# Performance work log

Hardware: AMD Instinct MI355X
Metric: run time of the kernel (lower is better)

## Reference

```python
import jax, jax.numpy as jnp
import numpy as np

# ---- static config (Phi-3-small layer 0, blocksparse branch) ----
HIDDEN = 4096
N_HEADS = 32
N_KV = 8
HEAD_DIM = HIDDEN // N_HEADS        # 128
Q_PER_KV = N_HEADS // N_KV          # 4
SEQ = 2048
ROPE_BASE = 1000000.0
POS_SCALE = 1.0
SM_SCALE = 1.0 / HEAD_DIM           # mup scaling, multiplier=1.0
BLOCK = 64
LOCAL_BLOCKS = 16
VERT_STRIDE = 8


def _blocksparse_mask(seq_len):
    """Dense [S,S] bool mask realizing the causal blocksparse pattern:
    query block i attends key block j iff j<=i and (i-j < LOCAL_BLOCKS or (j+1) % VERT_STRIDE == 0),
    with elementwise causality inside blocks. Built once in numpy (static)."""
    nb = seq_len // BLOCK
    qb = np.arange(nb)[:, None]
    kb = np.arange(nb)[None, :]
    bmask = (kb <= qb) & ((qb - kb < LOCAL_BLOCKS) | ((kb + 1) % VERT_STRIDE == 0))
    emask = np.kron(bmask, np.ones((BLOCK, BLOCK), dtype=bool))
    i = np.arange(seq_len)
    emask &= i[:, None] >= i[None, :]
    return jnp.asarray(emask)


def _rope(x, cos, sin):
    # x: [B, S, H, D]; cos/sin: [S, D]
    x1, x2 = jnp.split(x, 2, axis=-1)
    rot = jnp.concatenate([-x2, x1], axis=-1)
    return x * cos[None, :, None, :] + rot * sin[None, :, None, :]


def setup_inputs() -> dict:
    key = jax.random.key(0)
    k1, k2, k3, k4, k5 = jax.random.split(key, 5)
    qkv_out = (N_HEADS + 2 * N_KV) * HEAD_DIM  # 6144
    return {
        "hidden_states": jax.random.normal(k1, (1, SEQ, HIDDEN), dtype=jnp.float32),
        "w_qkv": jax.random.normal(k2, (qkv_out, HIDDEN), dtype=jnp.float32) * 0.02,
        "b_qkv": jnp.zeros((qkv_out,), dtype=jnp.float32),
        "w_dense": jax.random.normal(k3, (HIDDEN, HIDDEN), dtype=jnp.float32) * 0.02,
        "b_dense": jnp.zeros((HIDDEN,), dtype=jnp.float32),
    }


def reference(hidden_states, w_qkv, b_qkv, w_dense, b_dense):
    B, S, _ = hidden_states.shape
    # grouped QKV projection: [B,S,(H+2*KV)*D]
    qkv = jnp.einsum("bsh,oh->bso", hidden_states, w_qkv) + b_qkv
    # group layout: (group, q0..q3, k, v) per kv head
    qkv = qkv.reshape(B, S, N_KV, Q_PER_KV + 2, HEAD_DIM)
    q = qkv[:, :, :, :Q_PER_KV].reshape(B, S, N_HEADS, HEAD_DIM)
    k = qkv[:, :, :, Q_PER_KV]   # [B,S,KV,D]
    v = qkv[:, :, :, Q_PER_KV + 1]
    # rotary embeddings (HF rotate-half style)
    inv_freq = 1.0 / (ROPE_BASE ** (jnp.arange(0, HEAD_DIM, 2, dtype=jnp.float32) / HEAD_DIM))
    t = jnp.arange(S, dtype=jnp.float32) * POS_SCALE
    freqs = jnp.outer(t, inv_freq)               # [S, D/2]
    emb = jnp.concatenate([freqs, freqs], axis=-1)
    cos, sin = jnp.cos(emb), jnp.sin(emb)
    q = _rope(q, cos, sin)
    k = _rope(k, cos, sin)
    # GQA: replicate kv heads to match q heads
    k = jnp.repeat(k, Q_PER_KV, axis=2)          # [B,S,H,D]
    v = jnp.repeat(v, Q_PER_KV, axis=2)
    mask = _blocksparse_mask(S)                  # [S,S] bool
    scores = jnp.einsum("bqhd,bkhd->bhqk", q, k) * SM_SCALE
    scores = jnp.where(mask[None, None], scores, jnp.finfo(scores.dtype).min)
    probs = jax.nn.softmax(scores, axis=-1)
    ctx = jnp.einsum("bhqk,bkhd->bqhd", probs, v).reshape(B, S, HIDDEN)
    out = jnp.einsum("bsh,oh->bso", ctx, w_dense) + b_dense
    return out
```

## Files before the change

### kernel.cpp

```cpp
#include <hip/hip_runtime.h>
#include <hip/hip_bf16.h>

#define SEQ 2048
#define HIDDEN 4096
#define NH 32
#define NKV 8
#define HD 128
#define QKV_OUT 6144
#define QSCALE (0.0078125f * 1.4426950408889634f)

typedef __attribute__((ext_vector_type(8))) short bf16x8;
typedef __attribute__((ext_vector_type(4))) float f32x4;
typedef __attribute__((ext_vector_type(16))) float f32x16;

__device__ inline unsigned short f32_bf16(float f) {
  union { float f; unsigned int u; } v; v.f = f;
  unsigned int r = v.u + 0x7FFFu + ((v.u >> 16) & 1u);
  return (unsigned short)(r >> 16);
}
__device__ inline float bf16_f32(unsigned short u) {
  union { unsigned int u; float f; } v; v.u = (unsigned int)u << 16;
  return v.f;
}
__device__ inline unsigned int pk(float a, float b) {
  union { __hip_bfloat162 h; unsigned int u; } t;
  t.h = __float22bfloat162_rn(make_float2(a, b));
  return t.u;
}
__device__ inline void pswap(unsigned int &a, unsigned int &b) {
  auto r = __builtin_amdgcn_permlane32_swap((int)a, (int)b, false, false);
  a = (unsigned int)r[0]; b = (unsigned int)r[1];
}
__device__ inline float xmax32(float v) {
  int x = __builtin_bit_cast(int, v);
  auto r = __builtin_amdgcn_permlane32_swap(x, x, false, false);
  return fmaxf(__builtin_bit_cast(float, (int)r[0]), __builtin_bit_cast(float, (int)r[1]));
}
__device__ inline float xadd32(float v) {
  int x = __builtin_bit_cast(int, v);
  auto r = __builtin_amdgcn_permlane32_swap(x, x, false, false);
  return __builtin_bit_cast(float, (int)r[0]) + __builtin_bit_cast(float, (int)r[1]);
}

__global__ __launch_bounds__(256) void conv_bf16(const float* __restrict__ in,
                                                 unsigned short* __restrict__ out,
                                                 int n) {
  int i = (blockIdx.x * 256 + threadIdx.x) * 8;
  if (i + 8 > n) return;
  float4 a = *reinterpret_cast<const float4*>(in + i);
  float4 b = *reinterpret_cast<const float4*>(in + i + 4);
  unsigned short t[8];
  t[0] = f32_bf16(a.x); t[1] = f32_bf16(a.y); t[2] = f32_bf16(a.z); t[3] = f32_bf16(a.w);
  t[4] = f32_bf16(b.x); t[5] = f32_bf16(b.y); t[6] = f32_bf16(b.z); t[7] = f32_bf16(b.w);
  *reinterpret_cast<uint4*>(out + i) = *reinterpret_cast<uint4*>(t);
}

__global__ __launch_bounds__(256) void build_tab(float* __restrict__ ct,
                                                 float* __restrict__ st) {
  int idx = blockIdx.x * 256 + threadIdx.x;
  int s = idx >> 6, d = idx & 63;
  float inv = powf(1.0e6f, -(float)d * (1.0f / 64.0f));
  float f = (float)s * inv;
  ct[idx] = cosf(f);
  st[idx] = sinf(f);
}

template <int BM, int CR, int CC, bool OBF>
__global__ __launch_bounds__(512, 2) void gemmF(const unsigned short* __restrict__ A,
                                                const unsigned short* __restrict__ B,
                                                const float* __restrict__ bias,
                                                void* __restrict__ Cp,
                                                int M, int N, int K) {
  constexpr int BN = 256;
  constexpr int MQ = BM / 64;
  constexpr int ABYT = BM * 128;
  constexpr int SB = ABYT + 32768;
  constexpr int NA = BM / 64;
  __shared__ __align__(16) char Lds[SB * 2];

  const int tid = threadIdx.x;
  const int wave = tid >> 6, lane = tid & 63;
  const int wr = wave >> 2, wc = wave & 3;
  const int lrow = lane & 15, lgrp = lane >> 4;

  const int ntx = N / BN;
  const int wg0 = blockIdx.x;
  const int xcd = wg0 & 7, w = wg0 >> 3;
  const int cpb = ntx / CC;
  const int band = xcd / cpb, colc = xcd % cpb;
  const int bm = (band * CR + w / CC) * BM;
  const int bn = (colc * CC + w % CC) * BN;

  const int r8 = lane >> 3;
  const int scol = ((lane & 7) ^ r8) * 8;
  const unsigned short* gA[NA]; int lA[NA];
#pragma unroll
  for (int j = 0; j < NA; ++j) {
    int row = bm + wave * (BM / 8) + j * 8 + r8;
    gA[j] = A + (size_t)row * K + scol;
    lA[j] = wave * (BM / 8) * 128 + j * 1024;
  }
  const unsigned short* gB[4]; int lB[4];
#pragma unroll
  for (int j = 0; j < 4; ++j) {
    int row = bn + wave * 32 + j * 8 + r8;
    gB[j] = B + (size_t)row * K + scol;
    lB[j] = ABYT + wave * 32 * 128 + j * 1024;
  }

  auto stage = [&](int t) {
    const int bufb = (t & 1) * SB;
    const int k0 = t * 64;
#pragma unroll
    for (int j = 0; j < NA; ++j)
      __builtin_amdgcn_global_load_lds(
          (const __attribute__((address_space(1))) unsigned int*)(gA[j] + k0),
          (__attribute__((address_space(3))) unsigned int*)(Lds + bufb + lA[j]), 16, 0, 0);
#pragma unroll
    for (int j = 0; j < 4; ++j)
      __builtin_amdgcn_global_load_lds(
          (const __attribute__((address_space(1))) unsigned int*)(gB[j] + k0),
          (__attribute__((address_space(3))) unsigned int*)(Lds + bufb + lB[j]), 16, 0, 0);
  };

  const int rsw = (lrow & 7) << 4;
  auto aoff = [&](int mh, int m, int ks) {
    return (wr * (BM / 2) + mh * (BM / 4) + m * 16 + lrow) * 128 +
           ((ks * 64 + lgrp * 16) ^ rsw);
  };
  auto boff = [&](int nh, int n, int ks) {
    return ABYT + (wc * 64 + nh * 32 + n * 16 + lrow) * 128 +
           ((ks * 64 + lgrp * 16) ^ rsw);
  };

  f32x4 acc[2 * MQ][4] = {};
  bf16x8 af[MQ][2], bf0[2][2], bf1[2][2];
  const int nt = K / 64;

  stage(0);
  asm volatile("s_waitcnt vmcnt(0)" ::: "memory");
  __builtin_amdgcn_sched_barrier(0);
  __builtin_amdgcn_s_barrier();
  __builtin_amdgcn_sched_barrier(0);

  for (int t = 0; t < nt; ++t) {
    const char* base = Lds + (t & 1) * SB;
    const bool pf = (t + 1) < nt;

    if (pf) stage(t + 1);
#pragma unroll
    for (int m = 0; m < MQ; ++m)
#pragma unroll
      for (int ks = 0; ks < 2; ++ks)
        af[m][ks] = *reinterpret_cast<const bf16x8*>(base + aoff(0, m, ks));
#pragma unroll
    for (int n = 0; n < 2; ++n)
#pragma unroll
      for (int ks = 0; ks < 2; ++ks)
        bf0[n][ks] = *reinterpret_cast<const bf16x8*>(base + boff(0, n, ks));
    __builtin_amdgcn_s_barrier();
    asm volatile("s_waitcnt lgkmcnt(0)" ::: "memory");
    __builtin_amdgcn_sched_barrier(0);
    __builtin_amdgcn_s_setprio(1);
#pragma unroll
    for (int m = 0; m < MQ; ++m)
#pragma unroll
      for (int n = 0; n < 2; ++n)
#pragma unroll
        for (int ks = 0; ks < 2; ++ks)
          acc[m][n] = __builtin_amdgcn_mfma_f32_16x16x32_bf16(af[m][ks], bf0[n][ks], acc[m][n], 0, 0, 0);
    __builtin_amdgcn_s_setprio(0);
    __builtin_amdgcn_s_barrier();

#pragma unroll
    for (int n = 0; n < 2; ++n)
#pragma unroll
      for (int ks = 0; ks < 2; ++ks)
        bf1[n][ks] = *reinterpret_cast<const bf16x8*>(base + boff(1, n, ks));
    __builtin_amdgcn_s_barrier();
    asm volatile("s_waitcnt lgkmcnt(0)" ::: "memory");
    __builtin_amdgcn_sched_barrier(0);
    __builtin_amdgcn_s_setprio(1);
#pragma unroll
    for (int m = 0; m < MQ; ++m)
#pragma unroll
      for (int n = 0; n < 2; ++n)
#pragma unroll
        for (int ks = 0; ks < 2; ++ks)
          acc[m][2 + n] = __builtin_amdgcn_mfma_f32_16x16x32_bf16(af[m][ks], bf1[n][ks], acc[m][2 + n], 0, 0, 0);
    __builtin_amdgcn_s_setprio(0);
    __builtin_amdgcn_s_barrier();

#pragma unroll
    for (int m = 0; m < MQ; ++m)
#pragma unroll
      for (int ks = 0; ks < 2; ++ks)
        af[m][ks] = *reinterpret_cast<const bf16x8*>(base + aoff(1, m, ks));
    __builtin_amdgcn_s_barrier();
    asm volatile("s_waitcnt lgkmcnt(0)" ::: "memory");
    __builtin_amdgcn_sched_barrier(0);
    __builtin_amdgcn_s_setprio(1);
#pragma unroll
    for (int m = 0; m < MQ; ++m)
#pragma unroll
      for (int n = 0; n < 2; ++n)
#pragma unroll
        for (int ks = 0; ks < 2; ++ks)
          acc[MQ + m][n] = __builtin_amdgcn_mfma_f32_16x16x32_bf16(af[m][ks], bf0[n][ks], acc[MQ + m][n], 0, 0, 0);
    __builtin_amdgcn_s_setprio(0);
    __builtin_amdgcn_s_barrier();

    __builtin_amdgcn_s_setprio(1);
#pragma unroll
    for (int m = 0; m < MQ; ++m)
#pragma unroll
      for (int n = 0; n < 2; ++n)
#pragma unroll
        for (int ks = 0; ks < 2; ++ks)
          acc[MQ + m][2 + n] = __builtin_amdgcn_mfma_f32_16x16x32_bf16(af[m][ks], bf1[n][ks], acc[MQ + m][2 + n], 0, 0, 0);
    __builtin_amdgcn_s_setprio(0);
    if (pf) {
      asm volatile("s_waitcnt vmcnt(0)" ::: "memory");
      __builtin_amdgcn_sched_barrier(0);
      __builtin_amdgcn_s_barrier();
      __builtin_amdgcn_sched_barrier(0);
    }
  }

#pragma unroll
  for (int ni = 0; ni < 4; ++ni) {
    int col = bn + wc * 64 + ni * 16 + lrow;
    float bv = bias[col];
#pragma unroll
    for (int mi = 0; mi < 2 * MQ; ++mi)
#pragma unroll
      for (int r = 0; r < 4; ++r) {
        int row = bm + wr * (BM / 2) + mi * 16 + lgrp * 4 + r;
        if constexpr (OBF)
          ((unsigned short*)Cp)[(size_t)row * N + col] = f32_bf16(acc[mi][ni][r] + bv);
        else
          ((float*)Cp)[(size_t)row * N + col] = acc[mi][ni][r] + bv;
      }
  }
}

__global__ __launch_bounds__(256) void rope_split(const unsigned short* __restrict__ qkvb,
                                                  const float* __restrict__ ct,
                                                  const float* __restrict__ st,
                                                  unsigned short* __restrict__ Q,
                                                  unsigned short* __restrict__ Kh,
                                                  unsigned short* __restrict__ Vt) {
  int b = blockIdx.x;
  if (b < 5120) {
    int t = b * 256 + threadIdx.x;
    int d8 = (t & 15) * 8;
    int q = t >> 4;
    int s = q / 40;
    int slotg = q - s * 40;
    int g = slotg / 5, slot = slotg - g * 5;
    const unsigned short* base = qkvb + (size_t)s * QKV_OUT + g * 768 + slot * 128;
    bf16x8 x8 = *reinterpret_cast<const bf16x8*>(base + d8);
    bf16x8 r8 = *reinterpret_cast<const bf16x8*>(base + (d8 ^ 64));
    float4 c0 = *reinterpret_cast<const float4*>(ct + s * 64 + (d8 & 63));
    float4 c1 = *reinterpret_cast<const float4*>(ct + s * 64 + (d8 & 63) + 4);
    float4 s0 = *reinterpret_cast<const float4*>(st + s * 64 + (d8 & 63));
    float4 s1 = *reinterpret_cast<const float4*>(st + s * 64 + (d8 & 63) + 4);
    float cc[8] = {c0.x, c0.y, c0.z, c0.w, c1.x, c1.y, c1.z, c1.w};
    float ss[8] = {s0.x, s0.y, s0.z, s0.w, s1.x, s1.y, s1.z, s1.w};
    float sgn = (d8 < 64) ? -1.0f : 1.0f;
    float sc = (slot < 4) ? QSCALE : 1.0f;
    unsigned short o[8];
#pragma unroll
    for (int i = 0; i < 8; ++i) {
      float x = bf16_f32((unsigned short)x8[i]);
      float r = bf16_f32((unsigned short)r8[i]) * sgn;
      o[i] = f32_bf16((x * cc[i] + r * ss[i]) * sc);
    }
    unsigned short* dst = (slot < 4)
        ? Q + ((size_t)(g * 4 + slot) * SEQ + s) * HD + d8
        : Kh + ((size_t)g * SEQ + s) * HD + d8;
    *reinterpret_cast<uint4*>(dst) = *reinterpret_cast<uint4*>(o);
  } else {
    int t2 = (b - 5120) * 256 + threadIdx.x;
    int d = t2 & 127;
    int rest = t2 >> 7;
    int g = rest & 7;
    int s0 = (rest >> 3) * 8;
    const unsigned short* src = qkvb + (size_t)s0 * QKV_OUT + g * 768 + 640 + d;
    unsigned short o[8];
#pragma unroll
    for (int i = 0; i < 8; ++i) o[i] = src[(size_t)i * QKV_OUT];
    *reinterpret_cast<uint4*>(&Vt[((size_t)g * HD + d) * SEQ + s0]) =
        *reinterpret_cast<uint4*>(o);
  }
}

__device__ inline int nextj(int x, int qb) {
  if (x > qb) return -1;
  if (qb - x < 16) return x;
  int v = (x & ~7) + 7;
  int w = qb - 15;
  return v < w ? v : w;
}

__global__ __launch_bounds__(256, 2) void attn32(const unsigned short* __restrict__ Q,
                                                 const unsigned short* __restrict__ Kh,
                                                 const unsigned short* __restrict__ Vt,
                                                 unsigned short* __restrict__ ctx) {
  const int g = blockIdx.x;
  const int y = (int)gridDim.y - 1 - (int)blockIdx.y;
  const int qb = y >> 1, half = y & 1;
  const int Q0 = y * 32;
  const int tid = threadIdx.x;
  const int wave = tid >> 6;
  const int h = g * 4 + wave;
  const int lane = tid & 63;
  const int l31 = lane & 31, hi = lane >> 5;

  __shared__ __align__(16) char Lds[65536];

  auto stage = [&](int bufb, int j) {
#pragma unroll
    for (int i = 0; i < 4; ++i) {
      int row = i * 16 + (tid >> 4);
      const unsigned short* src =
          Kh + ((size_t)(g * SEQ + j * 64 + row)) * HD + ((tid & 15) ^ (row & 15)) * 8;
      __builtin_amdgcn_global_load_lds(
          (const __attribute__((address_space(1))) unsigned int*)src,
          (__attribute__((address_space(3))) unsigned int*)(Lds + bufb + i * 4096 + (tid >> 6) * 1024),
          16, 0, 0);
    }
#pragma unroll
    for (int i = 0; i < 4; ++i) {
      int row = i * 32 + (tid >> 3);
      const unsigned short* src =
          Vt + ((size_t)(g * HD + row)) * SEQ + j * 64 + ((tid & 7) ^ (row & 7)) * 8;
      __builtin_amdgcn_global_load_lds(
          (const __attribute__((address_space(1))) unsigned int*)src,
          (__attribute__((address_space(3))) unsigned int*)(Lds + bufb + 16384 + i * 4096 + (tid >> 6) * 1024),
          16, 0, 0);
    }
  };

  bf16x8 qf[8];
  const unsigned short* qbase = Q + ((size_t)h * SEQ + Q0 + l31) * HD;
#pragma unroll
  for (int kk = 0; kk < 8; ++kk)
    qf[kk] = *reinterpret_cast<const bf16x8*>(qbase + kk * 16 + hi * 8);

  f32x16 ot[4] = {};
  float mrow = -1e30f, lsum = 0.f;

  const int kswz = l31 & 15;
  const int vswz = l31 & 7;

  int j = nextj(0, qb);
  int cur = 0;
  stage(0, j);
  asm volatile("s_waitcnt vmcnt(0)" ::: "memory");
  __builtin_amdgcn_sched_barrier(0);
  __builtin_amdgcn_s_barrier();
  __builtin_amdgcn_sched_barrier(0);

  while (true) {
    const int jn = (j < qb) ? nextj(j + 1, qb) : -1;
    if (jn >= 0) stage(cur ^ 32768, jn);

    const char* kb = Lds + cur;
    const char* vb = Lds + cur + 16384;
    const bool diag = (j == qb);
    const bool short_blk = diag && (half == 0);

    f32x16 st[2] = {};
    __builtin_amdgcn_s_setprio(1);
#pragma unroll
    for (int kk = 0; kk < 8; ++kk) {
      bf16x8 k0 = *reinterpret_cast<const bf16x8*>(
          kb + (size_t)l31 * 256 + (((2 * kk + hi) ^ kswz) * 16));
      st[0] = __builtin_amdgcn_mfma_f32_32x32x16_bf16(k0, qf[kk], st[0], 0, 0, 0);
      if (!short_blk) {
        bf16x8 k1 = *reinterpret_cast<const bf16x8*>(
            kb + (size_t)(32 + l31) * 256 + (((2 * kk + hi) ^ kswz) * 16));
        st[1] = __builtin_amdgcn_mfma_f32_32x32x16_bf16(k1, qf[kk], st[1], 0, 0, 0);
      }
    }
    __builtin_amdgcn_s_setprio(0);

    if (diag) {
      int qrel = half * 32 + l31;
#pragma unroll
      for (int kt = 0; kt < 2; ++kt)
#pragma unroll
        for (int r = 0; r < 16; ++r) {
          int krel = kt * 32 + (r & 3) + 8 * (r >> 2) + 4 * hi;
          if (krel > qrel) st[kt][r] = -1e30f;
        }
    }

    float t16[16];
#pragma unroll
    for (int r = 0; r < 16; ++r) t16[r] = fmaxf(st[0][r], st[1][r]);
#pragma unroll
    for (int sft = 8; sft >= 1; sft >>= 1)
#pragma unroll
      for (int r = 0; r < sft; ++r) t16[r] = fmaxf(t16[r], t16[r + sft]);
    float vm = xmax32(t16[0]);

    if (!__all(vm - mrow <= 8.0f)) {
      float nm = fmaxf(mrow, vm);
      float corr = __builtin_amdgcn_exp2f(mrow - nm);
      lsum *= corr;
#pragma unroll
      for (int dt = 0; dt < 4; ++dt)
#pragma unroll
        for (int r = 0; r < 16; ++r) ot[dt][r] *= corr;
      mrow = nm;
    }

    float s4[4] = {0.f, 0.f, 0.f, 0.f};
#pragma unroll
    for (int kt = 0; kt < 2; ++kt)
#pragma unroll
      for (int r = 0; r < 16; ++r) {
        float p = __builtin_amdgcn_exp2f(st[kt][r] - mrow);
        st[kt][r] = p;
        s4[r & 3] += p;
      }
    lsum += xadd32((s4[0] + s4[1]) + (s4[2] + s4[3]));

    bf16x8 pb[4];
#pragma unroll
    for (int s = 0; s < 4; ++s) {
      int kt = s >> 1, g0 = (s & 1) * 2, g1 = g0 + 1;
      unsigned int a0 = pk(st[kt][4 * g0 + 0], st[kt][4 * g0 + 1]);
      unsigned int a1 = pk(st[kt][4 * g0 + 2], st[kt][4 * g0 + 3]);
      unsigned int b0 = pk(st[kt][4 * g1 + 0], st[kt][4 * g1 + 1]);
      unsigned int b1 = pk(st[kt][4 * g1 + 2], st[kt][4 * g1 + 3]);
      pswap(a0, b0);
      pswap(a1, b1);
      union { unsigned int u[4]; bf16x8 v; } t;
      t.u[0] = a0; t.u[1] = a1; t.u[2] = b0; t.u[3] = b1;
      pb[s] = t.v;
    }

    const int smax = short_blk ? 2 : 4;
    __builtin_amdgcn_s_setprio(1);
#pragma unroll
    for (int dt = 0; dt < 4; ++dt) {
      const char* vrow = vb + (size_t)(dt * 32 + l31) * 128;
#pragma unroll
      for (int s = 0; s < 4; ++s)
        if (s < smax)
          ot[dt] = __builtin_amdgcn_mfma_f32_32x32x16_bf16(
              *reinterpret_cast<const bf16x8*>(vrow + (((2 * s + hi) ^ vswz) * 16)),
              pb[s], ot[dt], 0, 0, 0);
    }
    __builtin_amdgcn_s_setprio(0);

    if (jn < 0) break;
    asm volatile("s_waitcnt vmcnt(0)" ::: "memory");
    __builtin_amdgcn_sched_barrier(0);
    __builtin_amdgcn_s_barrier();
    __builtin_amdgcn_sched_barrier(0);
    j = jn;
    cur ^= 32768;
  }

  __syncthreads();
  char* W = Lds + wave * 8192;
  float inv = 1.0f / lsum;
  const int swz = (l31 & 7) << 4;
#pragma unroll
  for (int dt = 0; dt < 4; ++dt)
#pragma unroll
    for (int gg = 0; gg < 4; ++gg) {
      unsigned int u0 = pk(ot[dt][4 * gg + 0] * inv, ot[dt][4 * gg + 1] * inv);
      unsigned int u1 = pk(ot[dt][4 * gg + 2] * inv, ot[dt][4 * gg + 3] * inv);
      int off = (dt * 64 + gg * 16 + hi * 8) ^ swz;
      *reinterpret_cast<uint2*>(W + l31 * 256 + off) = make_uint2(u0, u1);
    }
#pragma unroll
  for (int i = 0; i < 8; ++i) {
    int row = lane >> 1;
    int t = (lane & 1) * 8 + i;
    bf16x8 vv = *reinterpret_cast<const bf16x8*>(
        W + row * 256 + ((t * 16) ^ ((row & 7) << 4)));
    *reinterpret_cast<bf16x8*>(&ctx[(size_t)(Q0 + row) * HIDDEN + h * HD + t * 8]) = vv;
  }
}

extern "C" void kernel_launch(void* const* d_in, const int* in_sizes, int n_in,
                              void* d_out, int out_size, void* d_ws, size_t ws_size,
                              hipStream_t stream) {
  const float* hidden  = (const float*)d_in[0];
  const float* w_qkv   = (const float*)d_in[1];
  const float* b_qkv   = (const float*)d_in[2];
  const float* w_dense = (const float*)d_in[3];
  const float* b_dense = (const float*)d_in[4];
  float* out = (float*)d_out;

  char* p = (char*)d_ws;
  unsigned short* hid_bf  = (unsigned short*)p; p += (size_t)SEQ * HIDDEN * 2;
  unsigned short* wqkv_bf = (unsigned short*)p; p += (size_t)QKV_OUT * HIDDEN * 2;
  unsigned short* wd_bf   = (unsigned short*)p; p += (size_t)HIDDEN * HIDDEN * 2;
  unsigned short* qkvb    = (unsigned short*)p; p += (size_t)SEQ * QKV_OUT * 2;
  unsigned short* Qb      = (unsigned short*)p; p += (size_t)NH * SEQ * HD * 2;
  unsigned short* Kb      = (unsigned short*)p; p += (size_t)NKV * SEQ * HD * 2;
  unsigned short* Vt      = (unsigned short*)p; p += (size_t)NKV * HD * SEQ * 2;
  float* ct               = (float*)p;          p += (size_t)SEQ * 64 * 4;
  float* st               = (float*)p;          p += (size_t)SEQ * 64 * 4;
  unsigned short* ctx = hid_bf;

  conv_bf16<<<(SEQ * HIDDEN) / 2048, 256, 0, stream>>>(hidden, hid_bf, SEQ * HIDDEN);
  conv_bf16<<<(QKV_OUT * HIDDEN) / 2048, 256, 0, stream>>>(w_qkv, wqkv_bf, QKV_OUT * HIDDEN);
  conv_bf16<<<(HIDDEN * HIDDEN) / 2048, 256, 0, stream>>>(w_dense, wd_bf, HIDDEN * HIDDEN);
  build_tab<<<(SEQ * 64) / 256, 256, 0, stream>>>(ct, st);

  gemmF<256, 4, 6, true>
      <<<dim3((SEQ / 256) * (QKV_OUT / 256)), 512, 0, stream>>>(
          hid_bf, wqkv_bf, b_qkv, qkvb, SEQ, QKV_OUT, HIDDEN);
  rope_split<<<5120 + 1024, 256, 0, stream>>>(qkvb, ct, st, Qb, Kb, Vt);
  attn32<<<dim3(NKV, SEQ / 32), 256, 0, stream>>>(Qb, Kb, Vt, ctx);
  gemmF<128, 8, 4, false>
      <<<dim3((SEQ / 128) * (HIDDEN / 256)), 512, 0, stream>>>(
          ctx, wd_bf, b_dense, out, SEQ, HIDDEN, HIDDEN);
}
```

Measured before the change: 310.0 us.

## Fuse fp32-to-bf16 weight conversion into GEMM B-tile loading with register prefetch

Removes the two standalone weight conversion kernels. The GEMM now reads fp32 weights directly into registers two tiles ahead, packs them to bf16 and writes them into LDS, while A still uses direct global-to-LDS loads. The loop is restructured into even/odd register-buffered steps with one barrier per tile instead of several, and the QKV GEMM switches from 256-row to 128-row tiles. This avoids writing and re-reading bf16 weight copies, but doubles the global bytes read for B and adds register pressure and VALU packing inside the main loop.

```diff
diff --git a/kernel.cpp b/kernel.cpp
--- a/kernel.cpp
+++ b/kernel.cpp
@@ -65,13 +65,13 @@
   st[idx] = sinf(f);
 }
 
-template <int BM, int CR, int CC, bool OBF>
-__global__ __launch_bounds__(512, 2) void gemmF(const unsigned short* __restrict__ A,
-                                                const unsigned short* __restrict__ B,
+template <int CR, int CC, bool OBF>
+__global__ __launch_bounds__(512, 2) void gemmW(const unsigned short* __restrict__ A,
+                                                const float* __restrict__ B,
                                                 const float* __restrict__ bias,
                                                 void* __restrict__ Cp,
                                                 int M, int N, int K) {
-  constexpr int BN = 256;
+  constexpr int BM = 128, BN = 256;
   constexpr int MQ = BM / 64;
   constexpr int ABYT = BM * 128;
   constexpr int SB = ABYT + 32768;
@@ -91,36 +91,49 @@
   const int bm = (band * CR + w / CC) * BM;
   const int bn = (colc * CC + w % CC) * BN;
 
-  const int r8 = lane >> 3;
-  const int scol = ((lane & 7) ^ r8) * 8;
+  const int r8 = lane >> 3, c8 = lane & 7;
+  const int scolA = (c8 ^ r8) * 8;
   const unsigned short* gA[NA]; int lA[NA];
 #pragma unroll
   for (int j = 0; j < NA; ++j) {
     int row = bm + wave * (BM / 8) + j * 8 + r8;
-    gA[j] = A + (size_t)row * K + scol;
+    gA[j] = A + (size_t)row * K + scolA;
     lA[j] = wave * (BM / 8) * 128 + j * 1024;
   }
-  const unsigned short* gB[4]; int lB[4];
+  auto stageA = [&](int t) {
+    const int bufb = (t & 1) * SB;
+#pragma unroll
+    for (int j = 0; j < NA; ++j)
+      __builtin_amdgcn_global_load_lds(
+          (const __attribute__((address_space(1))) unsigned int*)(gA[j] + t * 64),
+          (__attribute__((address_space(3))) unsigned int*)(Lds + bufb + lA[j]), 16, 0, 0);
+  };
+
+  const float* gBs[4]; int lB[4];
 #pragma unroll
   for (int j = 0; j < 4; ++j) {
     int row = bn + wave * 32 + j * 8 + r8;
-    gB[j] = B + (size_t)row * K + scol;
-    lB[j] = ABYT + wave * 32 * 128 + j * 1024;
-  }
-
-  auto stage = [&](int t) {
-    const int bufb = (t & 1) * SB;
-    const int k0 = t * 64;
-#pragma unroll
-    for (int j = 0; j < NA; ++j)
-      __builtin_amdgcn_global_load_lds(
-          (const __attribute__((address_space(1))) unsigned int*)(gA[j] + k0),
-          (__attribute__((address_space(3))) unsigned int*)(Lds + bufb + lA[j]), 16, 0, 0);
-#pragma unroll
-    for (int j = 0; j < 4; ++j)
-      __builtin_amdgcn_global_load_lds(
-          (const __attribute__((address_space(1))) unsigned int*)(gB[j] + k0),
-          (__attribute__((address_space(3))) unsigned int*)(Lds + bufb + lB[j]), 16, 0, 0);
+    gBs[j] = B + (size_t)row * K + (c8 ^ r8) * 8;
+    lB[j] = ABYT + (wave * 32 + j * 8 + r8) * 128 + c8 * 16;
+  }
+  auto loadB = [&](f32x4 (&dst)[4][2], int t) {
+#pragma unroll
+    for (int j = 0; j < 4; ++j) {
+      dst[j][0] = *reinterpret_cast<const f32x4*>(gBs[j] + t * 64);
+      dst[j][1] = *reinterpret_cast<const f32x4*>(gBs[j] + t * 64 + 4);
+    }
+  };
+  auto writeB = [&](f32x4 (&src)[4][2], int t) {
+    char* bb = Lds + (t & 1) * SB;
+#pragma unroll
+    for (int j = 0; j < 4; ++j) {
+      uint4 u;
+      u.x = pk(src[j][0][0], src[j][0][1]);
+      u.y = pk(src[j][0][2], src[j][0][3]);
+      u.z = pk(src[j][1][0], src[j][1][1]);
+      u.w = pk(src[j][1][2], src[j][1][3]);
+      *reinterpret_cast<uint4*>(bb + lB[j]) = u;
+    }
   };
 
   const int rsw = (lrow & 7) << 4;
@@ -135,19 +148,31 @@
 
   f32x4 acc[2 * MQ][4] = {};
   bf16x8 af[MQ][2], bf0[2][2], bf1[2][2];
+  f32x4 bE[4][2], bO[4][2];
   const int nt = K / 64;
 
-  stage(0);
-  asm volatile("s_waitcnt vmcnt(0)" ::: "memory");
+  loadB(bE, 0);
+  stageA(0);
+  loadB(bO, 1);
+  asm volatile("s_waitcnt vmcnt(8)" ::: "memory");
   __builtin_amdgcn_sched_barrier(0);
-  __builtin_amdgcn_s_barrier();
+  writeB(bE, 0);
+  asm volatile("s_waitcnt lgkmcnt(0)" ::: "memory");
   __builtin_amdgcn_sched_barrier(0);
 
-  for (int t = 0; t < nt; ++t) {
+  auto tileStep = [&](int t, f32x4 (&wsrc)[4][2], f32x4 (&ldst)[4][2]) {
+    const bool pf1 = (t + 1) < nt, pf2 = (t + 2) < nt;
+    if (pf2) loadB(ldst, t + 2);
+    if (pf1) stageA(t + 1);
+    if (pf2)      asm volatile("s_waitcnt vmcnt(10) lgkmcnt(0)" ::: "memory");
+    else if (pf1) asm volatile("s_waitcnt vmcnt(2) lgkmcnt(0)" ::: "memory");
+    else          asm volatile("s_waitcnt vmcnt(0) lgkmcnt(0)" ::: "memory");
+    __builtin_amdgcn_sched_barrier(0);
+    __builtin_amdgcn_s_barrier();
+    __builtin_amdgcn_sched_barrier(0);
+    if (pf1) writeB(wsrc, t + 1);
+
     const char* base = Lds + (t & 1) * SB;
-    const bool pf = (t + 1) < nt;
-
-    if (pf) stage(t + 1);
 #pragma unroll
     for (int m = 0; m < MQ; ++m)
 #pragma unroll
@@ -158,9 +183,6 @@
 #pragma unroll
       for (int ks = 0; ks < 2; ++ks)
         bf0[n][ks] = *reinterpret_cast<const bf16x8*>(base + boff(0, n, ks));
-    __builtin_amdgcn_s_barrier();
-    asm volatile("s_waitcnt lgkmcnt(0)" ::: "memory");
-    __builtin_amdgcn_sched_barrier(0);
     __builtin_amdgcn_s_setprio(1);
 #pragma unroll
     for (int m = 0; m < MQ; ++m)
@@ -170,16 +192,11 @@
         for (int ks = 0; ks < 2; ++ks)
           acc[m][n] = __builtin_amdgcn_mfma_f32_16x16x32_bf16(af[m][ks], bf0[n][ks], acc[m][n], 0, 0, 0);
     __builtin_amdgcn_s_setprio(0);
-    __builtin_amdgcn_s_barrier();
-
 #pragma unroll
     for (int n = 0; n < 2; ++n)
 #pragma unroll
       for (int ks = 0; ks < 2; ++ks)
         bf1[n][ks] = *reinterpret_cast<const bf16x8*>(base + boff(1, n, ks));
-    __builtin_amdgcn_s_barrier();
-    asm volatile("s_waitcnt lgkmcnt(0)" ::: "memory");
-    __builtin_amdgcn_sched_barrier(0);
     __builtin_amdgcn_s_setprio(1);
 #pragma unroll
     for (int m = 0; m < MQ; ++m)
@@ -189,16 +206,11 @@
         for (int ks = 0; ks < 2; ++ks)
           acc[m][2 + n] = __builtin_amdgcn_mfma_f32_16x16x32_bf16(af[m][ks], bf1[n][ks], acc[m][2 + n], 0, 0, 0);
     __builtin_amdgcn_s_setprio(0);
-    __builtin_amdgcn_s_barrier();
-
 #pragma unroll
     for (int m = 0; m < MQ; ++m)
 #pragma unroll
       for (int ks = 0; ks < 2; ++ks)
         af[m][ks] = *reinterpret_cast<const bf16x8*>(base + aoff(1, m, ks));
-    __builtin_amdgcn_s_barrier();
-    asm volatile("s_waitcnt lgkmcnt(0)" ::: "memory");
-    __builtin_amdgcn_sched_barrier(0);
     __builtin_amdgcn_s_setprio(1);
 #pragma unroll
     for (int m = 0; m < MQ; ++m)
@@ -208,8 +220,6 @@
         for (int ks = 0; ks < 2; ++ks)
           acc[MQ + m][n] = __builtin_amdgcn_mfma_f32_16x16x32_bf16(af[m][ks], bf0[n][ks], acc[MQ + m][n], 0, 0, 0);
     __builtin_amdgcn_s_setprio(0);
-    __builtin_amdgcn_s_barrier();
-
     __builtin_amdgcn_s_setprio(1);
 #pragma unroll
     for (int m = 0; m < MQ; ++m)
@@ -219,12 +229,11 @@
         for (int ks = 0; ks < 2; ++ks)
           acc[MQ + m][2 + n] = __builtin_amdgcn_mfma_f32_16x16x32_bf16(af[m][ks], bf1[n][ks], acc[MQ + m][2 + n], 0, 0, 0);
     __builtin_amdgcn_s_setprio(0);
-    if (pf) {
-      asm volatile("s_waitcnt vmcnt(0)" ::: "memory");
-      __builtin_amdgcn_sched_barrier(0);
-      __builtin_amdgcn_s_barrier();
-      __builtin_amdgcn_sched_barrier(0);
-    }
+  };
+
+  for (int t = 0; t < nt; t += 2) {
+    tileStep(t, bO, bE);
+    tileStep(t + 1, bE, bO);
   }
 
 #pragma unroll
@@ -501,8 +510,6 @@
 
   char* p = (char*)d_ws;
   unsigned short* hid_bf  = (unsigned short*)p; p += (size_t)SEQ * HIDDEN * 2;
-  unsigned short* wqkv_bf = (unsigned short*)p; p += (size_t)QKV_OUT * HIDDEN * 2;
-  unsigned short* wd_bf   = (unsigned short*)p; p += (size_t)HIDDEN * HIDDEN * 2;
   unsigned short* qkvb    = (unsigned short*)p; p += (size_t)SEQ * QKV_OUT * 2;
   unsigned short* Qb      = (unsigned short*)p; p += (size_t)NH * SEQ * HD * 2;
   unsigned short* Kb      = (unsigned short*)p; p += (size_t)NKV * SEQ * HD * 2;
@@ -512,16 +519,14 @@
   unsigned short* ctx = hid_bf;
 
   conv_bf16<<<(SEQ * HIDDEN) / 2048, 256, 0, stream>>>(hidden, hid_bf, SEQ * HIDDEN);
-  conv_bf16<<<(QKV_OUT * HIDDEN) / 2048, 256, 0, stream>>>(w_qkv, wqkv_bf, QKV_OUT * HIDDEN);
-  conv_bf16<<<(HIDDEN * HIDDEN) / 2048, 256, 0, stream>>>(w_dense, wd_bf, HIDDEN * HIDDEN);
   build_tab<<<(SEQ * 64) / 256, 256, 0, stream>>>(ct, st);
 
-  gemmF<256, 4, 6, true>
-      <<<dim3((SEQ / 256) * (QKV_OUT / 256)), 512, 0, stream>>>(
-          hid_bf, wqkv_bf, b_qkv, qkvb, SEQ, QKV_OUT, HIDDEN);
+  gemmW<8, 6, true>
+      <<<dim3((SEQ / 128) * (QKV_OUT / 256)), 512, 0, stream>>>(
+          hid_bf, w_qkv, b_qkv, qkvb, SEQ, QKV_OUT, HIDDEN);
   rope_split<<<5120 + 1024, 256, 0, stream>>>(qkvb, ct, st, Qb, Kb, Vt);
   attn32<<<dim3(NKV, SEQ / 32), 256, 0, stream>>>(Qb, Kb, Vt, ctx);
-  gemmF<128, 8, 4, false>
+  gemmW<8, 4, false>
       <<<dim3((SEQ / 128) * (HIDDEN / 256)), 512, 0, stream>>>(
-          ctx, wd_bf, b_dense, out, SEQ, HIDDEN, HIDDEN);
-}
+          ctx, w_dense, b_dense, out, SEQ, HIDDEN, HIDDEN);
+}
```

New measurement: 350.6 us. +13.1%, slower.
